# Optimization experiments

Measured on AMD Instinct MI355X. Metric: run time of the kernel, lower is better.

The kernel has to match this reference:

```python
import jax, jax.numpy as jnp
import numpy as np

DN = ('NCHW', 'OIHW', 'NCHW')  # dimension numbers for all convs


def _dwconv(x, w, dim):
    # depthwise conv, valid padding; w: (dim,1,kh,kw)
    return jax.lax.conv_general_dilated(
        x, w, window_strides=(1, 1), padding='VALID',
        dimension_numbers=DN, feature_group_count=dim)


def setup_inputs() -> dict:
    key = jax.random.key(0)
    ks = jax.random.split(key, 5)
    B, C, H, W = 16, 256, 96, 96
    REP_K = 3
    x = jax.random.normal(ks[0], (B, C, H, W), dtype=jnp.float32)
    meta_pe = jax.random.normal(ks[1], (1, C, H, 1), dtype=jnp.float32) * 0.02
    weight = jax.random.normal(ks[2], (C, 1, H, 1), dtype=jnp.float32) * 0.02
    bias = jnp.zeros((C,), dtype=jnp.float32)
    rep_weight = jax.random.normal(ks[3], (C, 1, REP_K, 1), dtype=jnp.float32) * 0.02
    return {'x': x, 'meta_pe': meta_pe, 'weight': weight, 'bias': bias,
            'rep_weight': rep_weight}


def reference(x, meta_pe, weight, bias, rep_weight):
    # type == 'H': circular padding / conv along the H axis (kernels (K,1))
    dim = x.shape[1]
    rep_k = rep_weight.shape[2]
    # positional embedding add (broadcast over batch and W)
    x = x + meta_pe
    # local branch: circular pad by rep_k-1 rows, small depthwise conv
    x_cat = jnp.concatenate([x, x[:, :, :rep_k - 1, :]], axis=2)
    x_rep = _dwconv(x_cat, rep_weight, dim)
    # global branch: circular pad by H-1 rows, full-height depthwise conv + bias
    x_cat = jnp.concatenate([x, x[:, :, :-1, :]], axis=2)
    x_gcc = _dwconv(x_cat, weight, dim) + bias[None, :, None, None]
    return x_rep + x_gcc
```

## Files before the change

### kernel.cpp

```cpp
#include <hip/hip_runtime.h>

#define B_   16
#define C_   256
#define HH   96
#define WW   96
#define TPB  192

typedef _Float16 half8 __attribute__((ext_vector_type(8)));
typedef float   f32x16 __attribute__((ext_vector_type(16)));

__global__ __launch_bounds__(TPB, 4) void fused_circ_conv_mfma(
    const float* __restrict__ x,
    const float* __restrict__ meta_pe,
    const float* __restrict__ weight,
    const float* __restrict__ bias,
    const float* __restrict__ rep_weight,
    float* __restrict__ out)
{
    __shared__ float sW[2 * HH];
    __shared__ float sPE[HH];

    const int tid = threadIdx.x;
    const int blk = blockIdx.x;
    const int c   = blk & (C_ - 1);
    const size_t base = (size_t)blk * (HH * WW);

    {
        int k = (tid < HH) ? tid : (tid - HH);
        float wv = weight[c * HH + k];
        if (k < 3) wv += rep_weight[c * 3 + k];
        sW[tid] = wv;
        if (tid < HH) sPE[tid] = meta_pe[c * HH + tid];
    }
    __syncthreads();

    const int lane = tid & 63;
    const int wvid = tid >> 6;
    const int r32  = lane & 31;
    const int g    = lane >> 5;

    const float* __restrict__ xcol = x + base + (wvid * 32 + r32);
    float bx[48];
#pragma unroll
    for (int kt = 0; kt < 6; ++kt)
#pragma unroll
        for (int e = 0; e < 8; ++e)
            bx[kt * 8 + e] = xcol[(kt * 16 + g * 8 + e) * WW];

    half8 bh[6], bl[6];
#pragma unroll
    for (int kt = 0; kt < 6; ++kt) {
#pragma unroll
        for (int e = 0; e < 8; ++e) {
            float v = bx[kt * 8 + e] + sPE[kt * 16 + g * 8 + e];
            _Float16 h = (_Float16)v;
            bh[kt][e] = h;
            bl[kt][e] = (_Float16)(v - (float)h);
        }
    }

    const float bv = bias[c];

#pragma unroll 1
    for (int m = 0; m < 3; ++m) {
        f32x16 acc;
#pragma unroll
        for (int i = 0; i < 16; ++i) acc[i] = 0.f;

#pragma unroll
        for (int kt = 0; kt < 6; ++kt) {
            const float* wp = sW + (96 + kt * 16 + g * 8 - m * 32 - r32);
            half8 ah, al;
#pragma unroll
            for (int e = 0; e < 8; ++e) {
                float w_ = wp[e];
                _Float16 h = (_Float16)w_;
                ah[e] = h;
                al[e] = (_Float16)(w_ - (float)h);
            }
            acc = __builtin_amdgcn_mfma_f32_32x32x16_f16(ah, bh[kt], acc, 0, 0, 0);
            acc = __builtin_amdgcn_mfma_f32_32x32x16_f16(al, bh[kt], acc, 0, 0, 0);
            acc = __builtin_amdgcn_mfma_f32_32x32x16_f16(ah, bl[kt], acc, 0, 0, 0);
        }

        float* __restrict__ op = out + base + (wvid * 32 + r32);
#pragma unroll
        for (int reg = 0; reg < 16; ++reg) {
            int row = m * 32 + (reg & 3) + 8 * (reg >> 2) + 4 * g;
            op[row * WW] = acc[reg] + bv;
        }
    }
}

extern "C" void kernel_launch(void* const* d_in, const int* in_sizes, int n_in,
                              void* d_out, int out_size, void* d_ws, size_t ws_size,
                              hipStream_t stream) {
    const float* x          = (const float*)d_in[0];
    const float* meta_pe    = (const float*)d_in[1];
    const float* weight     = (const float*)d_in[2];
    const float* bias       = (const float*)d_in[3];
    const float* rep_weight = (const float*)d_in[4];
    float* out = (float*)d_out;

    fused_circ_conv_mfma<<<dim3(B_ * C_), dim3(TPB), 0, stream>>>(
        x, meta_pe, weight, bias, rep_weight, out);
}
```

Baseline: 267.1 us.

## Stage input through LDS with float4 loads and precompute circulant weight fragments

Each wave now loads its 96x32 input slab with coalesced float4 global loads, adds the positional embedding, and stores it to shared memory. MFMA B operands are then read from LDS instead of through strided scalar global loads. The six weight A-fragments (hi/lo split) are built once and reused across the three output row tiles via a circular index, and the m loop is fully unrolled. This raises register and LDS use and drops the occupancy hint from launch bounds, which may lower occupancy for a bandwidth-bound kernel.

```diff
diff --git a/kernel.cpp b/kernel.cpp
--- a/kernel.cpp
+++ b/kernel.cpp
@@ -9,7 +9,7 @@
 typedef _Float16 half8 __attribute__((ext_vector_type(8)));
 typedef float   f32x16 __attribute__((ext_vector_type(16)));
 
-__global__ __launch_bounds__(TPB, 4) void fused_circ_conv_mfma(
+__global__ __launch_bounds__(TPB) void fused_circ_conv_mfma(
     const float* __restrict__ x,
     const float* __restrict__ meta_pe,
     const float* __restrict__ weight,
@@ -17,77 +17,90 @@
     const float* __restrict__ rep_weight,
     float* __restrict__ out)
 {
+    __shared__ __align__(16) float sX[3][HH][32];
     __shared__ float sW[2 * HH];
-    __shared__ float sPE[HH];
 
-    const int tid = threadIdx.x;
-    const int blk = blockIdx.x;
-    const int c   = blk & (C_ - 1);
+    const int tid  = threadIdx.x;
+    const int blk  = blockIdx.x;
+    const int c    = blk & (C_ - 1);
     const size_t base = (size_t)blk * (HH * WW);
+
+    const int lane = tid & 63;
+    const int wv   = tid >> 6;
+    const int r32  = lane & 31;
+    const int g    = lane >> 5;
 
     {
         int k = (tid < HH) ? tid : (tid - HH);
-        float wv = weight[c * HH + k];
-        if (k < 3) wv += rep_weight[c * 3 + k];
-        sW[tid] = wv;
-        if (tid < HH) sPE[tid] = meta_pe[c * HH + tid];
+        float w_ = weight[c * HH + k];
+        if (k < 3) w_ += rep_weight[c * 3 + k];
+        sW[tid] = w_;
+    }
+
+    {
+        const int q  = lane & 7;
+        const int jr = lane >> 3;
+        const float* __restrict__ xg = x + base + wv * 32 + q * 4;
+        const float* __restrict__ pe = meta_pe + c * HH;
+        float* __restrict__ sxw = &sX[wv][0][0];
+#pragma unroll
+        for (int t = 0; t < 12; ++t) {
+            const int j = t * 8 + jr;
+            float4 v = *(const float4*)(xg + (size_t)j * WW);
+            float m = pe[j];
+            v.x += m; v.y += m; v.z += m; v.w += m;
+            *(float4*)(sxw + j * 32 + q * 4) = v;
+        }
     }
     __syncthreads();
 
-    const int lane = tid & 63;
-    const int wvid = tid >> 6;
-    const int r32  = lane & 31;
-    const int g    = lane >> 5;
-
-    const float* __restrict__ xcol = x + base + (wvid * 32 + r32);
-    float bx[48];
+    half8 ah[6], al[6];
 #pragma unroll
-    for (int kt = 0; kt < 6; ++kt)
+    for (int s = 0; s < 6; ++s) {
+        const float* wp = sW + (96 + s * 16 + g * 8 - r32);
 #pragma unroll
-        for (int e = 0; e < 8; ++e)
-            bx[kt * 8 + e] = xcol[(kt * 16 + g * 8 + e) * WW];
+        for (int e = 0; e < 8; ++e) {
+            float w_ = wp[e];
+            _Float16 h = (_Float16)w_;
+            ah[s][e] = h;
+            al[s][e] = (_Float16)(w_ - (float)h);
+        }
+    }
 
     half8 bh[6], bl[6];
+    {
+        const float* __restrict__ sxw = &sX[wv][0][0];
 #pragma unroll
-    for (int kt = 0; kt < 6; ++kt) {
+        for (int kt = 0; kt < 6; ++kt) {
 #pragma unroll
-        for (int e = 0; e < 8; ++e) {
-            float v = bx[kt * 8 + e] + sPE[kt * 16 + g * 8 + e];
-            _Float16 h = (_Float16)v;
-            bh[kt][e] = h;
-            bl[kt][e] = (_Float16)(v - (float)h);
+            for (int e = 0; e < 8; ++e) {
+                float v = sxw[(kt * 16 + g * 8 + e) * 32 + r32];
+                _Float16 h = (_Float16)v;
+                bh[kt][e] = h;
+                bl[kt][e] = (_Float16)(v - (float)h);
+            }
         }
     }
 
     const float bv = bias[c];
+    float* __restrict__ op = out + base + (wv * 32 + r32);
 
-#pragma unroll 1
+#pragma unroll
     for (int m = 0; m < 3; ++m) {
         f32x16 acc;
 #pragma unroll
         for (int i = 0; i < 16; ++i) acc[i] = 0.f;
-
 #pragma unroll
         for (int kt = 0; kt < 6; ++kt) {
-            const float* wp = sW + (96 + kt * 16 + g * 8 - m * 32 - r32);
-            half8 ah, al;
-#pragma unroll
-            for (int e = 0; e < 8; ++e) {
-                float w_ = wp[e];
-                _Float16 h = (_Float16)w_;
-                ah[e] = h;
-                al[e] = (_Float16)(w_ - (float)h);
-            }
-            acc = __builtin_amdgcn_mfma_f32_32x32x16_f16(ah, bh[kt], acc, 0, 0, 0);
-            acc = __builtin_amdgcn_mfma_f32_32x32x16_f16(al, bh[kt], acc, 0, 0, 0);
-            acc = __builtin_amdgcn_mfma_f32_32x32x16_f16(ah, bl[kt], acc, 0, 0, 0);
+            const int s = (kt + 6 - 2 * m) % 6;
+            acc = __builtin_amdgcn_mfma_f32_32x32x16_f16(ah[s], bh[kt], acc, 0, 0, 0);
+            acc = __builtin_amdgcn_mfma_f32_32x32x16_f16(al[s], bh[kt], acc, 0, 0, 0);
+            acc = __builtin_amdgcn_mfma_f32_32x32x16_f16(ah[s], bl[kt], acc, 0, 0, 0);
         }
-
-        float* __restrict__ op = out + base + (wvid * 32 + r32);
 #pragma unroll
         for (int reg = 0; reg < 16; ++reg) {
             int row = m * 32 + (reg & 3) + 8 * (reg >> 2) + 4 * g;
-            op[row * WW] = acc[reg] + bv;
+            op[(size_t)row * WW] = acc[reg] + bv;
         }
     }
 }
```

Measured after the change: 264.0 us. About the same (-1.2%).
